# Performance work log

Hardware: AMD Instinct MI355X
Metric: run time of the kernel (lower is better)

## Reference

```python
import jax, jax.numpy as jnp
import numpy as np

PACK = 8  # 32-bit words / 4-bit weights
GROUP = 128


def _unpack4(q):
    # q: [E, K//8, N] int32 packed nibbles -> [E, K, N] ints in [0, 15]
    nib = jnp.stack([(q >> (4 * j)) & 0xF for j in range(PACK)], axis=2)
    E, Kp, _, N = nib.shape
    return nib.reshape(E, Kp * PACK, N)


def _dequant(qweight, scales, g_idx):
    # GPTQ symmetric 4-bit: w = (nibble - 8) * scale[group(k), n]
    # g_idx (desc_act) maps each input row k to its quantization group,
    # equivalent math to Marlin's sorted-g_idx activation reordering.
    w = _unpack4(qweight).astype(jnp.float32) - 8.0          # [E, K, N]
    s = jnp.take_along_axis(scales, g_idx[:, :, None].astype(jnp.int32), axis=1)
    return w * s


def reference(x, router_logits, w13_qweight, w2_qweight,
              w13_scales, w2_scales, w13_g_idx, w2_g_idx, top_k):
    T = x.shape[0]
    E = w13_qweight.shape[0]
    W13 = _dequant(w13_qweight, w13_scales, w13_g_idx)   # [E, H, 2I]
    W2 = _dequant(w2_qweight, w2_scales, w2_g_idx)       # [E, I, H]
    I = W2.shape[1]

    # routing: softmax -> top-k -> renormalize
    probs = jax.nn.softmax(router_logits, axis=-1)       # [T, E]
    tw, tid = jax.lax.top_k(probs, top_k)                # [T, k]
    tw = tw / jnp.sum(tw, axis=-1, keepdims=True)
    cw = jnp.zeros((T, E), x.dtype).at[jnp.arange(T)[:, None], tid].add(tw)

    # grouped GEMM over all experts, weighted combine
    h = jnp.einsum('th,ehn->etn', x, W13)                # [E, T, 2I]
    gate, up = h[..., :I], h[..., I:]
    act = jax.nn.silu(gate) * up                         # [E, T, I]
    out_e = jnp.einsum('eti,eih->eth', act, W2)          # [E, T, H]
    return jnp.einsum('eth,te->th', out_e, cw)           # [T, H]


def setup_inputs() -> dict:
    key = jax.random.key(0)
    ks = jax.random.split(key, 8)
    T, E, H, I = 2048, 8, 1024, 4096
    x = jax.random.normal(ks[0], (T, H), dtype=jnp.float32)
    router_logits = jax.random.normal(ks[1], (T, E), dtype=jnp.float32)
    w13_qweight = jax.random.randint(ks[2], (E, H // PACK, 2 * I), 0, 2147483647, dtype=jnp.int32)
    w2_qweight = jax.random.randint(ks[3], (E, I // PACK, H), 0, 2147483647, dtype=jnp.int32)
    w13_scales = jax.random.uniform(ks[4], (E, H // GROUP, 2 * I), dtype=jnp.float32) * 0.02
    w2_scales = jax.random.uniform(ks[5], (E, I // GROUP, H), dtype=jnp.float32) * 0.02
    w13_g_idx = jax.random.randint(ks[6], (E, H), 0, H // GROUP, dtype=jnp.int32)
    w2_g_idx = jax.random.randint(ks[7], (E, I), 0, I // GROUP, dtype=jnp.int32)
    return {
        'x': x, 'router_logits': router_logits,
        'w13_qweight': w13_qweight, 'w2_qweight': w2_qweight,
        'w13_scales': w13_scales, 'w2_scales': w2_scales,
        'w13_g_idx': w13_g_idx, 'w2_g_idx': w2_g_idx,
        'top_k': 2,
    }
```

## Files before the change

kernel.cpp:

```cpp
#include <hip/hip_runtime.h>

#define T_TOK 2048
#define NEXP  8
#define H_DIM 1024
#define I_DIM 4096

#define N13  (2*I_DIM)
#define N2   (H_DIM)
#define NG13 8
#define NG2  32

#define KSPLIT2 4
#define KLEN2 (I_DIM/KSPLIT2)
#define BK   64

#define MAXT1 24

typedef __bf16 bf16x8 __attribute__((ext_vector_type(8)));
typedef float  f32x4  __attribute__((ext_vector_type(4)));

#define GLD_LDS(g, l) \
  __builtin_amdgcn_global_load_lds((const __attribute__((address_space(1))) void*)(g), \
                                   (__attribute__((address_space(3))) void*)(l), 16, 0, 0)

#define WS_OFFS   64
#define WS_PLIST  (WS_OFFS  + 64)
#define WS_PW     (WS_PLIST + 2*T_TOK*4)
#define WS_WL     65792
#define WS_NTS    66176
#define WS_SPOS   66432
#define PAIR_PAD  (2*T_TOK + 128)
#define WS_XG     131072
#define WS_ACT    (WS_XG  + PAIR_PAD*H_DIM*2)
#define WS_B1T    (WS_ACT + (size_t)PAIR_PAD*I_DIM*2)
#define WS_W2T    (WS_B1T + (size_t)NEXP*N13*H_DIM*2)

__global__ __launch_bounds__(512) void k_route(
    const float* __restrict__ logits,
    int* __restrict__ offs,
    int* __restrict__ plist, float* __restrict__ pw,
    int* __restrict__ spos,
    int* __restrict__ wl, int* __restrict__ nts) {

    __shared__ int cnt[NEXP], cur[NEXP];
    __shared__ short se[2*T_TOK];
    __shared__ float swt[2*T_TOK];

    const int tid = threadIdx.x;
    if (tid < NEXP) cnt[tid] = 0;
    __syncthreads();

    for (int t = tid; t < T_TOK; t += 512) {
        float l[NEXP];
        #pragma unroll
        for (int e = 0; e < NEXP; e++) l[e] = logits[t * NEXP + e];
        int i0 = 0; float b0 = l[0];
        #pragma unroll
        for (int e = 1; e < NEXP; e++) if (l[e] > b0) { b0 = l[e]; i0 = e; }
        int i1 = -1; float b1 = -1e30f;
        #pragma unroll
        for (int e = 0; e < NEXP; e++) if (e != i0 && l[e] > b1) { b1 = l[e]; i1 = e; }
        float w1 = 1.f / (1.f + __expf(b0 - b1));
        float w0 = 1.f - w1;
        se[2*t] = (short)i0; se[2*t+1] = (short)i1;
        swt[2*t] = w0; swt[2*t+1] = w1;
        atomicAdd(&cnt[i0], 1);
        atomicAdd(&cnt[i1], 1);
    }
    __syncthreads();

    if (tid == 0) {
        int s = 0;
        for (int e = 0; e < NEXP; e++) { offs[e] = s; cur[e] = s; s += cnt[e]; }
        offs[NEXP] = s;
        int n = 0;
        for (int e = 0; e < NEXP; e++)
            for (int mt = 0; mt * 256 < cnt[e]; mt++) wl[n++] = (e << 8) | mt;
        nts[0] = n;
    }
    __syncthreads();

    for (int t = tid; t < T_TOK; t += 512) {
        #pragma unroll
        for (int s = 0; s < 2; s++) {
            int e = se[2*t+s];
            int pos = atomicAdd(&cur[e], 1);
            plist[pos] = t;
            pw[pos] = swt[2*t+s];
            spos[2*t+s] = pos;
        }
    }
}

__global__ void k_gather(const float* __restrict__ x, const int* __restrict__ plist,
                         __bf16* __restrict__ xg) {
    int p = blockIdx.x;
    int t = plist[p];
    int i = threadIdx.x;
    const f32x4* src = reinterpret_cast<const f32x4*>(x + (size_t)t * H_DIM);
    f32x4 v0 = src[i*2], v1 = src[i*2+1];
    __align__(16) __bf16 tb[8];
    #pragma unroll
    for (int j = 0; j < 4; j++) { tb[j] = (__bf16)v0[j]; tb[4+j] = (__bf16)v1[j]; }
    *reinterpret_cast<f32x4*>(xg + (size_t)p * H_DIM + i*8) = *reinterpret_cast<f32x4*>(tb);
}

template<bool INTERLEAVE>
__global__ __launch_bounds__(256) void k_dequant(
    const int* __restrict__ q, const float* __restrict__ s, const int* __restrict__ g,
    __bf16* __restrict__ outw, int R, int K, int N, int NG) {

    const int e  = blockIdx.z;
    const int r0 = blockIdx.x * 64;
    const int k0 = blockIdx.y * 128;
    const int*   qe = q + (size_t)e * (K/8) * N;
    const float* se = s + (size_t)e * NG * N;
    const int*   ge = g + (size_t)e * K + k0;
    __bf16*      oe = outw + (size_t)e * R * K;

    __shared__ __align__(16) __bf16 tile[64][128];

    const int t  = threadIdx.x;
    const int rl = t & 63, kq = t >> 6;
    const int r  = r0 + rl;
    const int S  = INTERLEAVE ? (((r >> 4) << 3) + (r & 7) + (((r >> 3) & 1) ? (N >> 1) : 0))
                              : r;
    #pragma unroll
    for (int jj = 0; jj < 4; jj++) {
        int kp = kq + jj*4;
        int qv = qe[(size_t)(k0/8 + kp) * N + S];
        __align__(16) __bf16 tmp[8];
        #pragma unroll
        for (int j2 = 0; j2 < 8; j2++) {
            float sc = se[(size_t)ge[kp*8 + j2] * N + S];
            tmp[j2] = (__bf16)((float)(((qv >> (4*j2)) & 15) - 8) * sc);
        }
        int c = kp ^ (rl & 15);
        *reinterpret_cast<f32x4*>(&tile[rl][c*8]) = *reinterpret_cast<f32x4*>(tmp);
    }
    __syncthreads();
    #pragma unroll
    for (int i = 0; i < 4; i++) {
        int sidx = t + i*256;
        int row = sidx >> 4, ch = sidx & 15;
        int cs = ch ^ (row & 15);
        *reinterpret_cast<f32x4*>(oe + (size_t)(r0+row)*K + k0 + ch*8)
            = *reinterpret_cast<const f32x4*>(&tile[row][cs*8]);
    }
}

#define VM4 asm volatile("s_waitcnt vmcnt(4)" ::: "memory")
#define VM0 asm volatile("s_waitcnt vmcnt(0)" ::: "memory")
#define LGK0 { asm volatile("s_waitcnt lgkmcnt(0)" ::: "memory"); __builtin_amdgcn_sched_barrier(0); }
#define BARRIER  { __builtin_amdgcn_s_barrier(); __builtin_amdgcn_sched_barrier(0); }
#define SCHEDFENCE __builtin_amdgcn_sched_barrier(0)

__global__ __launch_bounds__(512) void k_gemm1(
    const __bf16* __restrict__ xg,
    const __bf16* __restrict__ B1t,
    const int*    __restrict__ offs,
    const float*  __restrict__ pw,
    const int*    __restrict__ wl,
    const int*    __restrict__ nts,
    __bf16*       __restrict__ act) {

    const int ti = blockIdx.x >> 5;
    if (ti >= nts[0]) return;
    const int nb = blockIdx.x & 31;
    const int w  = wl[ti];
    const int e  = w >> 8, mt = w & 255;
    const int m0 = offs[e] + mt * 256;
    const int mcount = min(offs[e+1] - m0, 256);
    const int n0r = nb * 256;

    __shared__ __align__(16) __bf16 AsF[2*2*8192];
    __shared__ __align__(16) __bf16 BsF[2*2*8192];
    __shared__ float wts[256];

    const int tid = threadIdx.x;
    const int wv = tid >> 6, lane = tid & 63;
    const int lrow = lane & 15, quad = lane >> 4;
    const int wr = (wv >> 2) * 128;
    const int wc = (wv & 3) * 64;
    const int cq = quad ^ ((lrow >> 1) & 3);

    for (int m = tid; m < 256; m += 512)
        wts[m] = (m < mcount) ? pw[m0 + m] : 0.f;

    const __bf16* Abase = xg  + (size_t)m0 * H_DIM;
    const __bf16* Bbase = B1t + ((size_t)e * N13 + n0r) * H_DIM;

    f32x4 acc[8][4];
    #pragma unroll
    for (int i = 0; i < 8; i++)
        #pragma unroll
        for (int j = 0; j < 4; j++) acc[i][j] = (f32x4)(0.f);

    auto stageA = [&](int prt, int h2, int kt) {
        const __bf16* g = Abase + kt * BK + h2 * 32;
        __bf16* d = AsF + prt * 16384 + h2 * 8192;
        #pragma unroll
        for (int q2 = 0; q2 < 2; q2++) {
            int row = (tid >> 2) + q2 * 128;
            int gch = (tid & 3) ^ ((row >> 1) & 3);
            int rowc = min(row, mcount - 1);
            GLD_LDS(g + (size_t)rowc * H_DIM + gch * 8, d + tid * 8 + q2 * 4096);
        }
    };
    auto stageB = [&](int prt, int h2, int kt) {
        const __bf16* g = Bbase + kt * BK + h2 * 32;
        __bf16* d = BsF + prt * 16384 + h2 * 8192;
        #pragma unroll
        for (int q2 = 0; q2 < 2; q2++) {
            int row = (tid >> 2) + q2 * 128;
            int gch = (tid & 3) ^ ((row >> 1) & 3);
            GLD_LDS(g + (size_t)row * H_DIM + gch * 8, d + tid * 8 + q2 * 4096);
        }
    };

    stageA(0, 0, 0); stageB(0, 0, 0); stageA(0, 1, 0); stageB(0, 1, 0);

    const int NT = H_DIM / BK;
    for (int kt = 0; kt < NT; kt++) {
        const int prt = kt & 1, nxt = prt ^ 1;
        const bool st = (kt + 1 < NT);
        const __bf16* Ab = AsF + prt * 16384;
        const __bf16* Bb = BsF + prt * 16384;
        #pragma unroll
        for (int h2 = 0; h2 < 2; h2++) {
            bf16x8 bb[4];
            if (h2 == 0) { VM4; } else if (st) { VM4; } else { VM0; }
            BARRIER;
            {
                #pragma unroll
                for (int j = 0; j < 4; j++)
                    bb[j] = *reinterpret_cast<const bf16x8*>(
                        &Bb[h2*8192 + (wc + 16*j + lrow)*32 + cq*8]);
                bf16x8 a[4];
                #pragma unroll
                for (int i = 0; i < 4; i++)
                    a[i] = *reinterpret_cast<const bf16x8*>(
                        &Ab[h2*8192 + (wr + 16*i + lrow)*32 + cq*8]);
                if (st) stageA(nxt, h2, kt + 1);
                LGK0;
                __builtin_amdgcn_s_setprio(1);
                #pragma unroll
                for (int j = 0; j < 4; j++)
                    #pragma unroll
                    for (int i = 0; i < 4; i++)
                        acc[i][j] = __builtin_amdgcn_mfma_f32_16x16x32_bf16(a[i], bb[j], acc[i][j], 0, 0, 0);
                __builtin_amdgcn_s_setprio(0);
            }
            SCHEDFENCE;
            BARRIER;
            {
                bf16x8 a[4];
                #pragma unroll
                for (int i = 0; i < 4; i++)
                    a[i] = *reinterpret_cast<const bf16x8*>(
                        &Ab[h2*8192 + (wr + 64 + 16*i + lrow)*32 + cq*8]);
                if (st) stageB(nxt, h2, kt + 1);
                LGK0;
                __builtin_amdgcn_s_setprio(1);
                #pragma unroll
                for (int j = 0; j < 4; j++)
                    #pragma unroll
                    for (int i = 0; i < 4; i++)
                        acc[4+i][j] = __builtin_amdgcn_mfma_f32_16x16x32_bf16(a[i], bb[j], acc[4+i][j], 0, 0, 0);
                __builtin_amdgcn_s_setprio(0);
            }
            SCHEDFENCE;
        }
    }

    #pragma unroll
    for (int j = 0; j < 4; j++) {
        const int c0 = ((n0r + wc + 16*j) >> 1);
        #pragma unroll
        for (int i = 0; i < 8; i++)
            #pragma unroll
            for (int rr = 0; rr < 4; rr++) {
                float v = acc[i][j][rr];
                float partner = __shfl_xor(v, 8, 64);
                int m = wr + 16*i + quad*4 + rr;
                if (lrow < 8 && m < mcount) {
                    float gg = v, uu = partner;
                    float a = (gg / (1.f + __expf(-gg))) * uu * wts[m];
                    act[(size_t)(m0 + m) * I_DIM + c0 + lrow] = (__bf16)a;
                }
            }
    }
}

__global__ __launch_bounds__(512) void k_gemm2(
    const __bf16* __restrict__ act,
    const __bf16* __restrict__ W2t,
    const int*    __restrict__ offs,
    const int*    __restrict__ wl,
    const int*    __restrict__ nts,
    float*        __restrict__ outp) {

    const int ti = blockIdx.x >> 4;
    if (ti >= nts[0]) return;
    const int nb = (blockIdx.x >> 2) & 3;
    const int ks = blockIdx.x & 3;
    const int w  = wl[ti];
    const int e  = w >> 8, mt = w & 255;
    const int m0 = offs[e] + mt * 256;
    const int mcount = min(offs[e+1] - m0, 256);
    const int n0 = nb * 256;
    const int kz = ks * KLEN2;

    __shared__ __align__(16) __bf16 AsF[2*2*8192];
    __shared__ __align__(16) __bf16 BsF[2*2*8192];

    const int tid = threadIdx.x;
    const int wv = tid >> 6, lane = tid & 63;
    const int lrow = lane & 15, quad = lane >> 4;
    const int wr = (wv >> 2) * 128;
    const int wc = (wv & 3) * 64;
    const int cq = quad ^ ((lrow >> 1) & 3);

    const __bf16* Abase = act + (size_t)m0 * I_DIM + kz;
    const __bf16* Bbase = W2t + ((size_t)e * N2 + n0) * I_DIM + kz;

    f32x4 acc[8][4];
    #pragma unroll
    for (int i = 0; i < 8; i++)
        #pragma unroll
        for (int j = 0; j < 4; j++) acc[i][j] = (f32x4)(0.f);

    auto stageA = [&](int prt, int h2, int kt) {
        const __bf16* g = Abase + kt * BK + h2 * 32;
        __bf16* d = AsF + prt * 16384 + h2 * 8192;
        #pragma unroll
        for (int q2 = 0; q2 < 2; q2++) {
            int row = (tid >> 2) + q2 * 128;
            int gch = (tid & 3) ^ ((row >> 1) & 3);
            int rowc = min(row, mcount - 1);
            GLD_LDS(g + (size_t)rowc * I_DIM + gch * 8, d + tid * 8 + q2 * 4096);
        }
    };
    auto stageB = [&](int prt, int h2, int kt) {
        const __bf16* g = Bbase + kt * BK + h2 * 32;
        __bf16* d = BsF + prt * 16384 + h2 * 8192;
        #pragma unroll
        for (int q2 = 0; q2 < 2; q2++) {
            int row = (tid >> 2) + q2 * 128;
            int gch = (tid & 3) ^ ((row >> 1) & 3);
            GLD_LDS(g + (size_t)row * I_DIM + gch * 8, d + tid * 8 + q2 * 4096);
        }
    };

    stageA(0, 0, 0); stageB(0, 0, 0); stageA(0, 1, 0); stageB(0, 1, 0);

    const int NT = KLEN2 / BK;
    for (int kt = 0; kt < NT; kt++) {
        const int prt = kt & 1, nxt = prt ^ 1;
        const bool st = (kt + 1 < NT);
        const __bf16* Ab = AsF + prt * 16384;
        const __bf16* Bb = BsF + prt * 16384;
        #pragma unroll
        for (int h2 = 0; h2 < 2; h2++) {
            bf16x8 bb[4];
            if (h2 == 0) { VM4; } else if (st) { VM4; } else { VM0; }
            BARRIER;
            {
                #pragma unroll
                for (int j = 0; j < 4; j++)
                    bb[j] = *reinterpret_cast<const bf16x8*>(
                        &Bb[h2*8192 + (wc + 16*j + lrow)*32 + cq*8]);
                bf16x8 a[4];
                #pragma unroll
                for (int i = 0; i < 4; i++)
                    a[i] = *reinterpret_cast<const bf16x8*>(
                        &Ab[h2*8192 + (wr + 16*i + lrow)*32 + cq*8]);
                if (st) stageA(nxt, h2, kt + 1);
                LGK0;
                __builtin_amdgcn_s_setprio(1);
                #pragma unroll
                for (int j = 0; j < 4; j++)
                    #pragma unroll
                    for (int i = 0; i < 4; i++)
                        acc[i][j] = __builtin_amdgcn_mfma_f32_16x16x32_bf16(a[i], bb[j], acc[i][j], 0, 0, 0);
                __builtin_amdgcn_s_setprio(0);
            }
            SCHEDFENCE;
            BARRIER;
            {
                bf16x8 a[4];
                #pragma unroll
                for (int i = 0; i < 4; i++)
                    a[i] = *reinterpret_cast<const bf16x8*>(
                        &Ab[h2*8192 + (wr + 64 + 16*i + lrow)*32 + cq*8]);
                if (st) stageB(nxt, h2, kt + 1);
                LGK0;
                __builtin_amdgcn_s_setprio(1);
                #pragma unroll
                for (int j = 0; j < 4; j++)
                    #pragma unroll
                    for (int i = 0; i < 4; i++)
                        acc[4+i][j] = __builtin_amdgcn_mfma_f32_16x16x32_bf16(a[i], bb[j], acc[4+i][j], 0, 0, 0);
                __builtin_amdgcn_s_setprio(0);
            }
            SCHEDFENCE;
        }
    }

    float* op = outp + ((size_t)ks * PAIR_PAD + m0) * N2;
    #pragma unroll
    for (int j = 0; j < 4; j++) {
        int h = n0 + wc + 16*j + lrow;
        #pragma unroll
        for (int i = 0; i < 8; i++)
            #pragma unroll
            for (int rr = 0; rr < 4; rr++) {
                int m = wr + 16*i + quad*4 + rr;
                if (m < mcount)
                    op[(size_t)m * N2 + h] = acc[i][j][rr];
            }
    }
}

__global__ __launch_bounds__(256) void k_reduce(
    const float* __restrict__ outp, const int* __restrict__ spos,
    float* __restrict__ out) {
    const int t  = blockIdx.x;
    const int h4 = threadIdx.x;
    const int p0 = spos[2*t], p1 = spos[2*t+1];
    const f32x4* r0 = reinterpret_cast<const f32x4*>(outp + (size_t)p0 * H_DIM) + h4;
    const f32x4* r1 = reinterpret_cast<const f32x4*>(outp + (size_t)p1 * H_DIM) + h4;
    f32x4 acc = (f32x4)(0.f);
    #pragma unroll
    for (int ks = 0; ks < KSPLIT2; ks++) {
        size_t off = (size_t)ks * (PAIR_PAD * (H_DIM/4));
        acc += r0[off] + r1[off];
    }
    reinterpret_cast<f32x4*>(out + (size_t)t * H_DIM)[h4] = acc;
}

extern "C" void kernel_launch(void* const* d_in, const int* in_sizes, int n_in,
                              void* d_out, int out_size, void* d_ws, size_t ws_size,
                              hipStream_t stream) {
    const float* x      = (const float*)d_in[0];
    const float* logits = (const float*)d_in[1];
    const int*   w13q   = (const int*)  d_in[2];
    const int*   w2q    = (const int*)  d_in[3];
    const float* w13s   = (const float*)d_in[4];
    const float* w2s    = (const float*)d_in[5];
    const int*   g13    = (const int*)  d_in[6];
    const int*   g2     = (const int*)  d_in[7];

    char* ws = (char*)d_ws;
    int*    offs   = (int*)   (ws + WS_OFFS);
    int*    plist  = (int*)   (ws + WS_PLIST);
    float*  pw     = (float*) (ws + WS_PW);
    int*    wl     = (int*)   (ws + WS_WL);
    int*    nts    = (int*)   (ws + WS_NTS);
    int*    spos   = (int*)   (ws + WS_SPOS);
    __bf16* xg     = (__bf16*)(ws + WS_XG);
    __bf16* act    = (__bf16*)(ws + WS_ACT);
    __bf16* B1t    = (__bf16*)(ws + WS_B1T);
    __bf16* W2t    = (__bf16*)(ws + WS_W2T);
    float*  outp   = (float*) (ws + WS_B1T);
    float*  out    = (float*) d_out;

    k_dequant<true ><<<dim3(N13/64, H_DIM/128, NEXP), 256, 0, stream>>>(
        w13q, w13s, g13, B1t, N13, H_DIM, N13, NG13);
    k_dequant<false><<<dim3(N2/64,  I_DIM/128, NEXP), 256, 0, stream>>>(
        w2q,  w2s,  g2,  W2t, N2,  I_DIM, N2,  NG2);

    k_route <<<1, 512, 0, stream>>>(logits, offs, plist, pw, spos, wl, nts);
    k_gather<<<2*T_TOK, 128, 0, stream>>>(x, plist, xg);

    k_gemm1<<<MAXT1 * 32, 512, 0, stream>>>(xg, B1t, offs, pw, wl, nts, act);
    k_gemm2<<<MAXT1 * 16, 512, 0, stream>>>(act, W2t, offs, wl, nts, outp);
    k_reduce<<<T_TOK, 256, 0, stream>>>(outp, spos, out);
}
```

Measured before the change: 389.1 us.

## Software-pipeline LDS fragment reads ahead of MFMA in both grouped GEMMs

Restructures the main k-loop of both expert GEMM kernels so the next LDS fragment reads are issued before each barrier and consumed in the following phase, instead of reading and then waiting right before the MFMAs. This lets LDS latency overlap with the previous phase's MFMA work. vmcnt waits are retuned to match the reordered global-to-LDS staging. The accumulators are split into low and high halves. The change adds more live fragment registers, which could increase register pressure, and the barrier placement has to stay correct for the double-buffered tiles.

New measurement: 395.5 us. About the same (+1.6%).

```diff
diff --git a/kernel.cpp b/kernel.cpp
--- a/kernel.cpp
+++ b/kernel.cpp
@@ -150,10 +150,28 @@
 }
 
 #define VM4 asm volatile("s_waitcnt vmcnt(4)" ::: "memory")
+#define VM2 asm volatile("s_waitcnt vmcnt(2)" ::: "memory")
 #define VM0 asm volatile("s_waitcnt vmcnt(0)" ::: "memory")
 #define LGK0 { asm volatile("s_waitcnt lgkmcnt(0)" ::: "memory"); __builtin_amdgcn_sched_barrier(0); }
 #define BARRIER  { __builtin_amdgcn_s_barrier(); __builtin_amdgcn_sched_barrier(0); }
 #define SCHEDFENCE __builtin_amdgcn_sched_barrier(0)
+
+#define MFMA16(ACC, A, B) \
+    { _Pragma("unroll") \
+      for (int j = 0; j < 4; j++) \
+        _Pragma("unroll") \
+        for (int i = 0; i < 4; i++) \
+            ACC[i][j] = __builtin_amdgcn_mfma_f32_16x16x32_bf16(A[i], B[j], ACC[i][j], 0, 0, 0); }
+
+#define READ_B(DST, BASE, KH) \
+    { _Pragma("unroll") \
+      for (int j = 0; j < 4; j++) \
+        DST[j] = *reinterpret_cast<const bf16x8*>(&(BASE)[(KH)*8192 + (wc + 16*j + lrow)*32 + cq*8]); }
+
+#define READ_A(DST, BASE, KH, RO) \
+    { _Pragma("unroll") \
+      for (int i = 0; i < 4; i++) \
+        DST[i] = *reinterpret_cast<const bf16x8*>(&(BASE)[(KH)*8192 + (wr + (RO) + 16*i + lrow)*32 + cq*8]); }
 
 __global__ __launch_bounds__(512) void k_gemm1(
     const __bf16* __restrict__ xg,
@@ -190,11 +208,11 @@
     const __bf16* Abase = xg  + (size_t)m0 * H_DIM;
     const __bf16* Bbase = B1t + ((size_t)e * N13 + n0r) * H_DIM;
 
-    f32x4 acc[8][4];
-    #pragma unroll
-    for (int i = 0; i < 8; i++)
-        #pragma unroll
-        for (int j = 0; j < 4; j++) acc[i][j] = (f32x4)(0.f);
+    f32x4 accL[4][4], accH[4][4];
+    #pragma unroll
+    for (int i = 0; i < 4; i++)
+        #pragma unroll
+        for (int j = 0; j < 4; j++) { accL[i][j] = (f32x4)(0.f); accH[i][j] = (f32x4)(0.f); }
 
     auto stageA = [&](int prt, int h2, int kt) {
         const __bf16* g = Abase + kt * BK + h2 * 32;
@@ -219,57 +237,60 @@
     };
 
     stageA(0, 0, 0); stageB(0, 0, 0); stageA(0, 1, 0); stageB(0, 1, 0);
+    VM4;
+    BARRIER;
+    bf16x8 bbA[4], bbB[4], aC[4], aN[4];
+    READ_B(bbA, BsF, 0);
+    READ_A(aC,  AsF, 0, 0);
+    SCHEDFENCE;
 
     const int NT = H_DIM / BK;
     for (int kt = 0; kt < NT; kt++) {
         const int prt = kt & 1, nxt = prt ^ 1;
         const bool st = (kt + 1 < NT);
-        const __bf16* Ab = AsF + prt * 16384;
-        const __bf16* Bb = BsF + prt * 16384;
-        #pragma unroll
-        for (int h2 = 0; h2 < 2; h2++) {
-            bf16x8 bb[4];
-            if (h2 == 0) { VM4; } else if (st) { VM4; } else { VM0; }
+        const __bf16* Ab  = AsF + prt * 16384;
+        const __bf16* Bb  = BsF + prt * 16384;
+        const __bf16* Abn = AsF + nxt * 16384;
+        const __bf16* Bbn = BsF + nxt * 16384;
+
+        LGK0;
+        __builtin_amdgcn_s_setprio(1);
+        MFMA16(accL, aC, bbA);
+        __builtin_amdgcn_s_setprio(0);
+        SCHEDFENCE;
+        if (st) { stageA(nxt, 0, kt + 1); VM2; } else { VM0; }
+        READ_A(aN, Ab, 0, 64);
+        BARRIER;
+
+        LGK0;
+        __builtin_amdgcn_s_setprio(1);
+        MFMA16(accH, aN, bbA);
+        __builtin_amdgcn_s_setprio(0);
+        SCHEDFENCE;
+        if (st) stageB(nxt, 0, kt + 1);
+        READ_B(bbB, Bb, 1);
+        READ_A(aC,  Ab, 1, 0);
+        BARRIER;
+
+        LGK0;
+        __builtin_amdgcn_s_setprio(1);
+        MFMA16(accL, aC, bbB);
+        __builtin_amdgcn_s_setprio(0);
+        SCHEDFENCE;
+        if (st) { stageA(nxt, 1, kt + 1); VM2; }
+        READ_A(aN, Ab, 1, 64);
+        BARRIER;
+
+        LGK0;
+        __builtin_amdgcn_s_setprio(1);
+        MFMA16(accH, aN, bbB);
+        __builtin_amdgcn_s_setprio(0);
+        SCHEDFENCE;
+        if (st) {
+            stageB(nxt, 1, kt + 1);
+            READ_B(bbA, Bbn, 0);
+            READ_A(aC,  Abn, 0, 0);
             BARRIER;
-            {
-                #pragma unroll
-                for (int j = 0; j < 4; j++)
-                    bb[j] = *reinterpret_cast<const bf16x8*>(
-                        &Bb[h2*8192 + (wc + 16*j + lrow)*32 + cq*8]);
-                bf16x8 a[4];
-                #pragma unroll
-                for (int i = 0; i < 4; i++)
-                    a[i] = *reinterpret_cast<const bf16x8*>(
-                        &Ab[h2*8192 + (wr + 16*i + lrow)*32 + cq*8]);
-                if (st) stageA(nxt, h2, kt + 1);
-                LGK0;
-                __builtin_amdgcn_s_setprio(1);
-                #pragma unroll
-                for (int j = 0; j < 4; j++)
-                    #pragma unroll
-                    for (int i = 0; i < 4; i++)
-                        acc[i][j] = __builtin_amdgcn_mfma_f32_16x16x32_bf16(a[i], bb[j], acc[i][j], 0, 0, 0);
-                __builtin_amdgcn_s_setprio(0);
-            }
-            SCHEDFENCE;
-            BARRIER;
-            {
-                bf16x8 a[4];
-                #pragma unroll
-                for (int i = 0; i < 4; i++)
-                    a[i] = *reinterpret_cast<const bf16x8*>(
-                        &Ab[h2*8192 + (wr + 64 + 16*i + lrow)*32 + cq*8]);
-                if (st) stageB(nxt, h2, kt + 1);
-                LGK0;
-                __builtin_amdgcn_s_setprio(1);
-                #pragma unroll
-                for (int j = 0; j < 4; j++)
-                    #pragma unroll
-                    for (int i = 0; i < 4; i++)
-                        acc[4+i][j] = __builtin_amdgcn_mfma_f32_16x16x32_bf16(a[i], bb[j], acc[4+i][j], 0, 0, 0);
-                __builtin_amdgcn_s_setprio(0);
-            }
-            SCHEDFENCE;
         }
     }
 
@@ -280,7 +301,7 @@
         for (int i = 0; i < 8; i++)
             #pragma unroll
             for (int rr = 0; rr < 4; rr++) {
-                float v = acc[i][j][rr];
+                float v = (i < 4) ? accL[i][j][rr] : accH[i-4][j][rr];
                 float partner = __shfl_xor(v, 8, 64);
                 int m = wr + 16*i + quad*4 + rr;
                 if (lrow < 8 && m < mcount) {
@@ -324,11 +345,11 @@
     const __bf16* Abase = act + (size_t)m0 * I_DIM + kz;
     const __bf16* Bbase = W2t + ((size_t)e * N2 + n0) * I_DIM + kz;
 
-    f32x4 acc[8][4];
-    #pragma unroll
-    for (int i = 0; i < 8; i++)
-        #pragma unroll
-        for (int j = 0; j < 4; j++) acc[i][j] = (f32x4)(0.f);
+    f32x4 accL[4][4], accH[4][4];
+    #pragma unroll
+    for (int i = 0; i < 4; i++)
+        #pragma unroll
+        for (int j = 0; j < 4; j++) { accL[i][j] = (f32x4)(0.f); accH[i][j] = (f32x4)(0.f); }
 
     auto stageA = [&](int prt, int h2, int kt) {
         const __bf16* g = Abase + kt * BK + h2 * 32;
@@ -353,57 +374,60 @@
     };
 
     stageA(0, 0, 0); stageB(0, 0, 0); stageA(0, 1, 0); stageB(0, 1, 0);
+    VM4;
+    BARRIER;
+    bf16x8 bbA[4], bbB[4], aC[4], aN[4];
+    READ_B(bbA, BsF, 0);
+    READ_A(aC,  AsF, 0, 0);
+    SCHEDFENCE;
 
     const int NT = KLEN2 / BK;
     for (int kt = 0; kt < NT; kt++) {
         const int prt = kt & 1, nxt = prt ^ 1;
         const bool st = (kt + 1 < NT);
-        const __bf16* Ab = AsF + prt * 16384;
-        const __bf16* Bb = BsF + prt * 16384;
-        #pragma unroll
-        for (int h2 = 0; h2 < 2; h2++) {
-            bf16x8 bb[4];
-            if (h2 == 0) { VM4; } else if (st) { VM4; } else { VM0; }
+        const __bf16* Ab  = AsF + prt * 16384;
+        const __bf16* Bb  = BsF + prt * 16384;
+        const __bf16* Abn = AsF + nxt * 16384;
+        const __bf16* Bbn = BsF + nxt * 16384;
+
+        LGK0;
+        __builtin_amdgcn_s_setprio(1);
+        MFMA16(accL, aC, bbA);
+        __builtin_amdgcn_s_setprio(0);
+        SCHEDFENCE;
+        if (st) { stageA(nxt, 0, kt + 1); VM2; } else { VM0; }
+        READ_A(aN, Ab, 0, 64);
+        BARRIER;
+
+        LGK0;
+        __builtin_amdgcn_s_setprio(1);
+        MFMA16(accH, aN, bbA);
+        __builtin_amdgcn_s_setprio(0);
+        SCHEDFENCE;
+        if (st) stageB(nxt, 0, kt + 1);
+        READ_B(bbB, Bb, 1);
+        READ_A(aC,  Ab, 1, 0);
+        BARRIER;
+
+        LGK0;
+        __builtin_amdgcn_s_setprio(1);
+        MFMA16(accL, aC, bbB);
+        __builtin_amdgcn_s_setprio(0);
+        SCHEDFENCE;
+        if (st) { stageA(nxt, 1, kt + 1); VM2; }
+        READ_A(aN, Ab, 1, 64);
+        BARRIER;
+
+        LGK0;
+        __builtin_amdgcn_s_setprio(1);
+        MFMA16(accH, aN, bbB);
+        __builtin_amdgcn_s_setprio(0);
+        SCHEDFENCE;
+        if (st) {
+            stageB(nxt, 1, kt + 1);
+            READ_B(bbA, Bbn, 0);
+            READ_A(aC,  Abn, 0, 0);
             BARRIER;
-            {
-                #pragma unroll
-                for (int j = 0; j < 4; j++)
-                    bb[j] = *reinterpret_cast<const bf16x8*>(
-                        &Bb[h2*8192 + (wc + 16*j + lrow)*32 + cq*8]);
-                bf16x8 a[4];
-                #pragma unroll
-                for (int i = 0; i < 4; i++)
-                    a[i] = *reinterpret_cast<const bf16x8*>(
-                        &Ab[h2*8192 + (wr + 16*i + lrow)*32 + cq*8]);
-                if (st) stageA(nxt, h2, kt + 1);
-                LGK0;
-                __builtin_amdgcn_s_setprio(1);
-                #pragma unroll
-                for (int j = 0; j < 4; j++)
-                    #pragma unroll
-                    for (int i = 0; i < 4; i++)
-                        acc[i][j] = __builtin_amdgcn_mfma_f32_16x16x32_bf16(a[i], bb[j], acc[i][j], 0, 0, 0);
-                __builtin_amdgcn_s_setprio(0);
-            }
-            SCHEDFENCE;
-            BARRIER;
-            {
-                bf16x8 a[4];
-                #pragma unroll
-                for (int i = 0; i < 4; i++)
-                    a[i] = *reinterpret_cast<const bf16x8*>(
-                        &Ab[h2*8192 + (wr + 64 + 16*i + lrow)*32 + cq*8]);
-                if (st) stageB(nxt, h2, kt + 1);
-                LGK0;
-                __builtin_amdgcn_s_setprio(1);
-                #pragma unroll
-                for (int j = 0; j < 4; j++)
-                    #pragma unroll
-                    for (int i = 0; i < 4; i++)
-                        acc[4+i][j] = __builtin_amdgcn_mfma_f32_16x16x32_bf16(a[i], bb[j], acc[4+i][j], 0, 0, 0);
-                __builtin_amdgcn_s_setprio(0);
-            }
-            SCHEDFENCE;
         }
     }
 
@@ -416,8 +440,9 @@
             #pragma unroll
             for (int rr = 0; rr < 4; rr++) {
                 int m = wr + 16*i + quad*4 + rr;
+                float v = (i < 4) ? accL[i][j][rr] : accH[i-4][j][rr];
                 if (m < mcount)
-                    op[(size_t)m * N2 + h] = acc[i][j][rr];
+                    op[(size_t)m * N2 + h] = v;
             }
     }
 }
```
